# Optimization experiments

Measured on AMD Instinct MI355X. Metric: run time of the kernel, lower is better.

Reference implementation:

```python
import jax, jax.numpy as jnp
import numpy as np

IN_DIM, HID, NCLS = 384, 16, 2
BN_EPS = 1e-5

def setup_inputs() -> dict:
    key = jax.random.key(0)
    ks = jax.random.split(key, 10)
    N, E, G = 50000, 200000, 64
    x = jax.random.normal(ks[0], (N, IN_DIM), dtype=jnp.float32)
    edge_index = jax.random.randint(ks[1], (2, E), 0, N, dtype=jnp.int64)
    batch = jnp.sort(jax.random.randint(ks[2], (N,), 0, G, dtype=jnp.int64))
    s1 = 1.0 / np.sqrt(2 * IN_DIM)
    s2 = 1.0 / np.sqrt(IN_DIM)
    s3 = 1.0 / np.sqrt(HID)
    lin_l_w = jax.random.uniform(ks[3], (HID, 2 * IN_DIM), minval=-s1, maxval=s1, dtype=jnp.float32)
    lin_l_b = jax.random.uniform(ks[4], (HID,), minval=-s1, maxval=s1, dtype=jnp.float32)
    lin_r_w = jax.random.uniform(ks[5], (HID, IN_DIM), minval=-s2, maxval=s2, dtype=jnp.float32)
    bn_gamma = jnp.ones((HID,), dtype=jnp.float32)
    bn_beta = jnp.zeros((HID,), dtype=jnp.float32)
    fc_w = jax.random.uniform(ks[6], (NCLS, HID), minval=-s3, maxval=s3, dtype=jnp.float32)
    fc_b = jax.random.uniform(ks[7], (NCLS,), minval=-s3, maxval=s3, dtype=jnp.float32)
    return {"x": x, "edge_index": edge_index, "batch": batch, "num_graphs": G,
            "lin_l_w": lin_l_w, "lin_l_b": lin_l_b, "lin_r_w": lin_r_w,
            "bn_gamma": bn_gamma, "bn_beta": bn_beta, "fc_w": fc_w, "fc_b": fc_b}

def reference(x, edge_index, batch, num_graphs, lin_l_w, lin_l_b, lin_r_w, bn_gamma, bn_beta, fc_w, fc_b):
    N = x.shape[0]
    # flow='target_to_source': aggregate x[edge_index[1]] (j) onto edge_index[0] (i)
    i, j = edge_index[0], edge_index[1]
    msg = x[j]                                                    # [E, IN_DIM]
    sum_agg = jax.ops.segment_sum(msg, i, num_segments=N)        # [N, IN_DIM]
    cnt = jax.ops.segment_sum(jnp.ones((msg.shape[0],), x.dtype), i, num_segments=N)
    mean_agg = sum_agg / jnp.clip(cnt, 1.0)[:, None]
    max_agg = jax.ops.segment_max(msg, i, num_segments=N)        # -inf where empty
    max_agg = jnp.where(jnp.isfinite(max_agg), max_agg, 0.0)     # PyG leaves 0 for isolated nodes
    agg = jnp.concatenate([mean_agg, max_agg], axis=-1)          # [N, 2*IN_DIM] (MultiAggregation cat)
    h = agg @ lin_l_w.T + lin_l_b + x @ lin_r_w.T                # SAGEConv: lin_l(aggr) + lin_r(root)
    # BatchNorm1d, training-mode batch statistics (biased variance)
    mu = jnp.mean(h, axis=0)
    var = jnp.mean(jnp.square(h - mu), axis=0)
    h = (h - mu) * jax.lax.rsqrt(var + BN_EPS) * bn_gamma + bn_beta
    h = jax.nn.relu(h)                                           # [N, HID]; hierarchical cat of 1 layer = h
    # global_mean_pool
    pooled_sum = jax.ops.segment_sum(h, batch, num_segments=num_graphs)
    gcnt = jax.ops.segment_sum(jnp.ones((N,), h.dtype), batch, num_segments=num_graphs)
    pooled = pooled_sum / jnp.clip(gcnt, 1.0)[:, None]           # [G, HID]
    return pooled @ fc_w.T + fc_b                                # [G, NCLS]
```

## Files before the change

### kernel.cpp

```cpp
#include <hip/hip_runtime.h>
#include <hip/hip_bf16.h>
#include <math.h>

#define IN_DIM 384
#define HID 16
#define NCLS 2
#define BN_EPS 1e-5f
#define MAXG 64
#define SLOTS 64

#define LOF(u) __uint_as_float((u) << 16)
#define HIF(u) __uint_as_float((u) & 0xffff0000u)

typedef __attribute__((ext_vector_type(8))) short bf16x8;
typedef __attribute__((ext_vector_type(4))) float f32x4;

__device__ __forceinline__ unsigned packbf(float a, float b) {
    __hip_bfloat162 h2 = __float22bfloat162_rn(make_float2(a, b));
    union { __hip_bfloat162 h; unsigned u; } c;
    c.h = h2;
    return c.u;
}

__global__ __launch_bounds__(256) void k_scatproj(const int* __restrict__ ei,
                                                  const int* __restrict__ ej, int E,
                                                  int* __restrict__ cnt,
                                                  int* __restrict__ colidx, int sblocks,
                                                  const float* __restrict__ x,
                                                  const float* __restrict__ wl,
                                                  const float* __restrict__ wr,
                                                  int N, float* __restrict__ y,
                                                  unsigned* __restrict__ xb) {
    if ((int)blockIdx.x < sblocks) {
        int e = blockIdx.x * 256 + threadIdx.x;
        if (e < E) {
            int i = ei[e];
            int pos = atomicAdd(&cnt[i], 1);
            if (pos < SLOTS) colidx[(size_t)i * SLOTS + pos] = ej[e];
        }
        return;
    }
    int lane = threadIdx.x & 63;
    int tile = (blockIdx.x - sblocks) * 4 + (threadIdx.x >> 6);
    int ntiles = (N + 15) >> 4;
    if (tile >= ntiles) return;
    int row = lane & 15;
    int g = lane >> 4;
    int node = tile * 16 + row;
    int nodec = min(node, N - 1);
    bool ok = (node < N);
    const float* xr = x + (size_t)nodec * IN_DIM + g * 8;
    const float* wmr = wl + (size_t)row * (2 * IN_DIM) + g * 8;
    const float* wrr = wr + (size_t)row * IN_DIM + g * 8;
    uint4* xo = (uint4*)(xb + (size_t)nodec * 192 + g * 4);
    f32x4 acc0 = {0.f, 0.f, 0.f, 0.f};
    f32x4 acc1 = {0.f, 0.f, 0.f, 0.f};
#pragma unroll
    for (int c = 0; c < 12; c++) {
        float4 xa = *(const float4*)(xr + c * 32);
        float4 xc = *(const float4*)(xr + c * 32 + 4);
        float4 ma = *(const float4*)(wmr + c * 32);
        float4 mc = *(const float4*)(wmr + c * 32 + 4);
        float4 ra = *(const float4*)(wrr + c * 32);
        float4 rc = *(const float4*)(wrr + c * 32 + 4);
        union { uint4 u; bf16x8 v; } xf, wa, wb;
        xf.u.x = packbf(xa.x, xa.y);
        xf.u.y = packbf(xa.z, xa.w);
        xf.u.z = packbf(xc.x, xc.y);
        xf.u.w = packbf(xc.z, xc.w);
        wa.u.x = packbf(ma.x, ma.y);
        wa.u.y = packbf(ma.z, ma.w);
        wa.u.z = packbf(mc.x, mc.y);
        wa.u.w = packbf(mc.z, mc.w);
        wb.u.x = packbf(ra.x, ra.y);
        wb.u.y = packbf(ra.z, ra.w);
        wb.u.z = packbf(rc.x, rc.y);
        wb.u.w = packbf(rc.z, rc.w);
        if (ok) xo[c * 4] = xf.u;
        acc0 = __builtin_amdgcn_mfma_f32_16x16x32_bf16(wa.v, xf.v, acc0, 0, 0, 0);
        acc1 = __builtin_amdgcn_mfma_f32_16x16x32_bf16(wb.v, xf.v, acc1, 0, 0, 0);
    }
    if (ok) {
        float* yo = y + (size_t)node * 32 + g * 4;
        *(float4*)yo = make_float4(acc0[0], acc0[1], acc0[2], acc0[3]);
        *(float4*)(yo + 16) = make_float4(acc1[0], acc1[1], acc1[2], acc1[3]);
    }
}

__global__ __launch_bounds__(256) void k_node(const unsigned* __restrict__ xb,
                                              const float* __restrict__ y,
                                              const float* __restrict__ wl,
                                              const float* __restrict__ lb,
                                              const int* __restrict__ cnt,
                                              const int* __restrict__ colidx, int N,
                                              float* __restrict__ h,
                                              float* __restrict__ stats) {
    __shared__ float shS[32];
    if (threadIdx.x < 32) shS[threadIdx.x] = 0.f;
    __syncthreads();
    int lane = threadIdx.x & 63;
    int wid = threadIdx.x >> 6;
    int kq = ((lane >> 4) << 2) + (lane & 3);
    int nq = (lane & 15) >> 2;
    int slot = lane >> 4;
    int ch = lane & 15;
    float sAcc = 0.f, s2Acc = 0.f;
    int ngroups = (N + 3) >> 2;
    int g = blockIdx.x * 4 + wid;
    if (g < ngroups) {
        int ibase = g << 2;
        int jpre[4];
        int dgv[4];
#pragma unroll
        for (int n = 0; n < 4; n++) {
            int i = ibase + n;
            dgv[n] = (i < N) ? min(cnt[i], SLOTS) : 0;
        }
#pragma unroll
        for (int n = 0; n < 4; n++) {
            int i = ibase + n;
            jpre[n] = (dgv[n] > 0) ? colidx[(size_t)i * SLOTS + min(lane, dgv[n] - 1)] : 0;
        }
        float2 mx[4][3];
        float sd[4];
#pragma unroll
        for (int n = 0; n < 4; n++) {
            int dg = dgv[n];
            float2 m0 = make_float2(-INFINITY, -INFINITY), m1 = m0, m2 = m0;
            float s = 0.f;
            int jv = jpre[n];
            for (int eb = 0; eb < dg; eb += 4) {
                int j0 = __shfl(jv, eb, 64);
                int j1 = __shfl(jv, eb + 1, 64);
                int j2 = __shfl(jv, eb + 2, 64);
                int j3 = __shfl(jv, eb + 3, 64);
                const unsigned* q0 = xb + (size_t)j0 * 192 + lane;
                const unsigned* q1 = xb + (size_t)j1 * 192 + lane;
                const unsigned* q2 = xb + (size_t)j2 * 192 + lane;
                const unsigned* q3 = xb + (size_t)j3 * 192 + lane;
                unsigned a0 = q0[0], a1 = q0[64], a2 = q0[128];
                unsigned b0 = q1[0], b1 = q1[64], b2 = q1[128];
                unsigned c0 = q2[0], c1 = q2[64], c2 = q2[128];
                unsigned d0 = q3[0], d1 = q3[64], d2 = q3[128];
                int js = (slot == 0) ? j0 : (slot == 1) ? j1 : (slot == 2) ? j2 : j3;
                float yv = y[(size_t)js * 32 + ch];
                s += (eb + slot < dg) ? yv : 0.f;
                m0.x = fmaxf(fmaxf(m0.x, fmaxf(LOF(a0), LOF(b0))), fmaxf(LOF(c0), LOF(d0)));
                m0.y = fmaxf(fmaxf(m0.y, fmaxf(HIF(a0), HIF(b0))), fmaxf(HIF(c0), HIF(d0)));
                m1.x = fmaxf(fmaxf(m1.x, fmaxf(LOF(a1), LOF(b1))), fmaxf(LOF(c1), LOF(d1)));
                m1.y = fmaxf(fmaxf(m1.y, fmaxf(HIF(a1), HIF(b1))), fmaxf(HIF(c1), HIF(d1)));
                m2.x = fmaxf(fmaxf(m2.x, fmaxf(LOF(a2), LOF(b2))), fmaxf(LOF(c2), LOF(d2)));
                m2.y = fmaxf(fmaxf(m2.y, fmaxf(HIF(a2), HIF(b2))), fmaxf(HIF(c2), HIF(d2)));
            }
            if (dgv[n] == 0) {
                m0 = make_float2(0.f, 0.f); m1 = m0; m2 = m0;
            }
            mx[n][0] = m0; mx[n][1] = m1; mx[n][2] = m2;
            sd[n] = s;
        }
#pragma unroll
        for (int n = 0; n < 4; n++) {
            sd[n] += __shfl_xor(sd[n], 16, 64);
            sd[n] += __shfl_xor(sd[n], 32, 64);
        }
        const float* wp = wl + IN_DIM + 2 * lane;
        float outv = 0.f;
#pragma unroll
        for (int kg = 0; kg < 4; kg++) {
            float r[16];
#pragma unroll
            for (int kk = 0; kk < 4; kk++) {
                int k = (kg << 2) + kk;
                const float* wrow = wp + (size_t)k * (2 * IN_DIM);
                float2 w0 = *(const float2*)wrow;
                float2 w1 = *(const float2*)(wrow + 128);
                float2 w2 = *(const float2*)(wrow + 256);
#pragma unroll
                for (int n = 0; n < 4; n++) {
                    float t = mx[n][0].x * w0.x;
                    t = fmaf(mx[n][0].y, w0.y, t);
                    t = fmaf(mx[n][1].x, w1.x, t);
                    t = fmaf(mx[n][1].y, w1.y, t);
                    t = fmaf(mx[n][2].x, w2.x, t);
                    t = fmaf(mx[n][2].y, w2.y, t);
                    r[(n << 2) + kk] = t;
                }
            }
#pragma unroll
            for (int st = 0; st < 4; st++) {
                int step = 1 << st;
                bool hi = (lane & step) != 0;
#pragma unroll
                for (int m = 0; m < (8 >> st); m++) {
                    float a = r[2 * m], b = r[2 * m + 1];
                    float send = hi ? a : b;
                    float keep = hi ? b : a;
                    r[m] = keep + __shfl_xor(send, step, 64);
                }
            }
            float v = r[0];
            v += __shfl_xor(v, 16, 64);
            v += __shfl_xor(v, 32, 64);
            if ((lane >> 4) == kg) outv = v;
        }
        int iw = ibase + nq;
        float t0 = __shfl(sd[0], kq, 64), t1 = __shfl(sd[1], kq, 64);
        float t2 = __shfl(sd[2], kq, 64), t3 = __shfl(sd[3], kq, 64);
        float sv = (nq == 0) ? t0 : (nq == 1) ? t1 : (nq == 2) ? t2 : t3;
        int dgs = (nq == 0) ? dgv[0] : (nq == 1) ? dgv[1] : (nq == 2) ? dgv[2] : dgv[3];
        if (iw < N) {
            float mean = sv / (float)max(dgs, 1);
            float hv = mean + outv + y[(size_t)iw * 32 + 16 + kq] + lb[kq];
            h[(size_t)iw * HID + kq] = hv;
            sAcc += hv;
            s2Acc = fmaf(hv, hv, s2Acc);
        }
    }
    __syncthreads();
    atomicAdd(&shS[kq], sAcc);
    atomicAdd(&shS[16 + kq], s2Acc);
    __syncthreads();
    if (threadIdx.x < 32) atomicAdd(&stats[threadIdx.x], shS[threadIdx.x]);
}

__global__ __launch_bounds__(256) void k_pool(const float* __restrict__ h,
                                              const int* __restrict__ batch,
                                              const float* __restrict__ stats,
                                              const float* __restrict__ gamma,
                                              const float* __restrict__ beta, int N,
                                              float* __restrict__ pooled,
                                              int* __restrict__ gcnt,
                                              int* __restrict__ ticket,
                                              const float* __restrict__ fcw,
                                              const float* __restrict__ fcb, int G,
                                              float* __restrict__ out) {
    __shared__ float smP[MAXG * HID];
    __shared__ int smC[MAXG];
    __shared__ int isLast;
    for (int idx = threadIdx.x; idx < MAXG * HID; idx += blockDim.x) smP[idx] = 0.f;
    if (threadIdx.x < MAXG) smC[threadIdx.x] = 0;
    __syncthreads();
    int c = threadIdx.x & 15;
    float invN = 1.f / (float)N;
    float mu = stats[c] * invN;
    float var = stats[16 + c] * invN - mu * mu;
    float sc = gamma[c] * rsqrtf(var + BN_EPS);
    float sh = beta[c] - mu * sc;
    int base = blockIdx.x * 256;
    int endn = min(base + 256, N);
    for (int idx = base * HID + threadIdx.x; idx < endn * HID; idx += blockDim.x) {
        int n = idx >> 4;
        float v = fmaxf(fmaf(h[idx], sc, sh), 0.f);
        int g = batch[n] & (MAXG - 1);
        atomicAdd(&smP[g * HID + c], v);
        if (c == 0) atomicAdd(&smC[g], 1);
    }
    __syncthreads();
    for (int idx = threadIdx.x; idx < MAXG * HID; idx += blockDim.x)
        if (smP[idx] != 0.f) atomicAdd(&pooled[idx], smP[idx]);
    if (threadIdx.x < MAXG && smC[threadIdx.x]) atomicAdd(&gcnt[threadIdx.x], smC[threadIdx.x]);
    __threadfence();
    __syncthreads();
    if (threadIdx.x == 0) {
        int t = atomicAdd(ticket, 1);
        isLast = (t == (int)gridDim.x - 1);
    }
    __syncthreads();
    if (isLast && threadIdx.x < G) {
        int g = threadIdx.x;
        __threadfence();
        int cntg = atomicAdd(&gcnt[g], 0);
        float inv = 1.f / (float)max(cntg, 1);
        float o0 = fcb[0], o1 = fcb[1];
#pragma unroll
        for (int chh = 0; chh < HID; chh++) {
            float pv = atomicAdd(&pooled[g * HID + chh], 0.f) * inv;
            o0 = fmaf(pv, fcw[chh], o0);
            o1 = fmaf(pv, fcw[HID + chh], o1);
        }
        out[g * NCLS + 0] = o0;
        out[g * NCLS + 1] = o1;
    }
}

extern "C" void kernel_launch(void* const* d_in, const int* in_sizes, int n_in,
                              void* d_out, int out_size, void* d_ws, size_t ws_size,
                              hipStream_t stream) {
    const float* x = (const float*)d_in[0];
    const int* ei = (const int*)d_in[1];
    const int* batch = (const int*)d_in[2];
    const float* wl = (const float*)d_in[4];
    const float* lb = (const float*)d_in[5];
    const float* wr = (const float*)d_in[6];
    const float* gamma = (const float*)d_in[7];
    const float* beta = (const float*)d_in[8];
    const float* fcw = (const float*)d_in[9];
    const float* fcb = (const float*)d_in[10];

    const int N = in_sizes[0] / IN_DIM;
    const int E = in_sizes[1] / 2;
    const int G = out_size / NCLS;
    const int* ej = ei + E;

    size_t off = 0;
    auto take = [&](size_t b) { size_t r = off; off += (b + 255) & ~(size_t)255; return r; };
    size_t cnt_off  = take((size_t)N * 4);
    size_t stat_off = take(32 * 4);
    size_t pool_off = take((size_t)MAXG * HID * 4);
    size_t gcnt_off = take((size_t)MAXG * 4);
    size_t tick_off = take(4);
    size_t zero_bytes = off;
    size_t col_off  = take((size_t)N * SLOTS * 4);
    size_t y_off    = take((size_t)N * 32 * 4);
    size_t h_off    = take((size_t)N * HID * 4);
    size_t xb_off   = take((size_t)N * 192 * 4 + 4096);
    (void)ws_size;

    char* ws = (char*)d_ws;
    int* cnt = (int*)(ws + cnt_off);
    float* stats = (float*)(ws + stat_off);
    float* pooled = (float*)(ws + pool_off);
    int* gcnt = (int*)(ws + gcnt_off);
    int* ticket = (int*)(ws + tick_off);
    int* colidx = (int*)(ws + col_off);
    float* y = (float*)(ws + y_off);
    float* h = (float*)(ws + h_off);
    unsigned* xb = (unsigned*)(ws + xb_off);

    hipMemsetAsync(d_ws, 0, zero_bytes, stream);

    int eblocks = (E + 255) / 256;
    int ngroups = (N + 3) >> 2;
    int gblocks = (ngroups + 3) / 4;
    int ntiles = (N + 15) >> 4;
    int pblocks = (ntiles + 3) / 4;
    k_scatproj<<<eblocks + pblocks, 256, 0, stream>>>(ei, ej, E, cnt, colidx, eblocks,
                                                      x, wl, wr, N, y, xb);
    k_node<<<gblocks, 256, 0, stream>>>(xb, y, wl, lb, cnt, colidx, N, h, stats);
    k_pool<<<(N + 255) / 256, 256, 0, stream>>>(h, batch, stats, gamma, beta, N, pooled,
                                                gcnt, ticket, fcw, fcb, G, (float*)d_out);
}
```

Baseline: 140.1 us.

## Drop bf16 copy of x; gather fp32 rows directly for max aggregation

Removes the bf16 staging buffer of x that the projection kernel wrote, so the neighbor max-gather in k_node now reads fp32 rows of x directly. The projection kernel now handles two 16-node tiles per wave, reusing the converted weight fragments across both tiles. This removes a 38MB write and the extra launch-side buffer, but doubles the bytes read per gathered neighbor (fp32 instead of bf16), trading write traffic for heavier random gather traffic.

```diff
diff --git a/kernel.cpp b/kernel.cpp
--- a/kernel.cpp
+++ b/kernel.cpp
@@ -8,9 +8,6 @@
 #define BN_EPS 1e-5f
 #define MAXG 64
 #define SLOTS 64
-
-#define LOF(u) __uint_as_float((u) << 16)
-#define HIF(u) __uint_as_float((u) & 0xffff0000u)
 
 typedef __attribute__((ext_vector_type(8))) short bf16x8;
 typedef __attribute__((ext_vector_type(4))) float f32x4;
@@ -29,8 +26,7 @@
                                                   const float* __restrict__ x,
                                                   const float* __restrict__ wl,
                                                   const float* __restrict__ wr,
-                                                  int N, float* __restrict__ y,
-                                                  unsigned* __restrict__ xb) {
+                                                  int N, float* __restrict__ y) {
     if ((int)blockIdx.x < sblocks) {
         int e = blockIdx.x * 256 + threadIdx.x;
         if (e < E) {
@@ -41,53 +37,60 @@
         return;
     }
     int lane = threadIdx.x & 63;
-    int tile = (blockIdx.x - sblocks) * 4 + (threadIdx.x >> 6);
     int ntiles = (N + 15) >> 4;
-    if (tile >= ntiles) return;
+    int npairs = (ntiles + 1) >> 1;
+    int pair = (blockIdx.x - sblocks) * 4 + (threadIdx.x >> 6);
+    if (pair >= npairs) return;
+    int t0 = pair * 2;
+    int t1 = min(t0 + 1, ntiles - 1);
+    bool two = (t0 + 1 < ntiles);
     int row = lane & 15;
     int g = lane >> 4;
-    int node = tile * 16 + row;
-    int nodec = min(node, N - 1);
-    bool ok = (node < N);
-    const float* xr = x + (size_t)nodec * IN_DIM + g * 8;
+    int node0 = t0 * 16 + row, node1 = t1 * 16 + row;
+    int nc0 = min(node0, N - 1), nc1 = min(node1, N - 1);
+    bool ok0 = (node0 < N), ok1 = two && (node1 < N);
+    const float* xr0 = x + (size_t)nc0 * IN_DIM + g * 8;
+    const float* xr1 = x + (size_t)nc1 * IN_DIM + g * 8;
     const float* wmr = wl + (size_t)row * (2 * IN_DIM) + g * 8;
     const float* wrr = wr + (size_t)row * IN_DIM + g * 8;
-    uint4* xo = (uint4*)(xb + (size_t)nodec * 192 + g * 4);
-    f32x4 acc0 = {0.f, 0.f, 0.f, 0.f};
-    f32x4 acc1 = {0.f, 0.f, 0.f, 0.f};
+    f32x4 a0m = {0.f, 0.f, 0.f, 0.f}, a0r = a0m, a1m = a0m, a1r = a0m;
 #pragma unroll
     for (int c = 0; c < 12; c++) {
-        float4 xa = *(const float4*)(xr + c * 32);
-        float4 xc = *(const float4*)(xr + c * 32 + 4);
         float4 ma = *(const float4*)(wmr + c * 32);
         float4 mc = *(const float4*)(wmr + c * 32 + 4);
         float4 ra = *(const float4*)(wrr + c * 32);
         float4 rc = *(const float4*)(wrr + c * 32 + 4);
-        union { uint4 u; bf16x8 v; } xf, wa, wb;
-        xf.u.x = packbf(xa.x, xa.y);
-        xf.u.y = packbf(xa.z, xa.w);
-        xf.u.z = packbf(xc.x, xc.y);
-        xf.u.w = packbf(xc.z, xc.w);
-        wa.u.x = packbf(ma.x, ma.y);
-        wa.u.y = packbf(ma.z, ma.w);
-        wa.u.z = packbf(mc.x, mc.y);
-        wa.u.w = packbf(mc.z, mc.w);
-        wb.u.x = packbf(ra.x, ra.y);
-        wb.u.y = packbf(ra.z, ra.w);
-        wb.u.z = packbf(rc.x, rc.y);
-        wb.u.w = packbf(rc.z, rc.w);
-        if (ok) xo[c * 4] = xf.u;
-        acc0 = __builtin_amdgcn_mfma_f32_16x16x32_bf16(wa.v, xf.v, acc0, 0, 0, 0);
-        acc1 = __builtin_amdgcn_mfma_f32_16x16x32_bf16(wb.v, xf.v, acc1, 0, 0, 0);
-    }
-    if (ok) {
-        float* yo = y + (size_t)node * 32 + g * 4;
-        *(float4*)yo = make_float4(acc0[0], acc0[1], acc0[2], acc0[3]);
-        *(float4*)(yo + 16) = make_float4(acc1[0], acc1[1], acc1[2], acc1[3]);
-    }
-}
-
-__global__ __launch_bounds__(256) void k_node(const unsigned* __restrict__ xb,
+        float4 p0 = *(const float4*)(xr0 + c * 32);
+        float4 q0 = *(const float4*)(xr0 + c * 32 + 4);
+        float4 p1 = *(const float4*)(xr1 + c * 32);
+        float4 q1 = *(const float4*)(xr1 + c * 32 + 4);
+        union { uint4 u; bf16x8 v; } wa, wb, x0, x1;
+        wa.u.x = packbf(ma.x, ma.y); wa.u.y = packbf(ma.z, ma.w);
+        wa.u.z = packbf(mc.x, mc.y); wa.u.w = packbf(mc.z, mc.w);
+        wb.u.x = packbf(ra.x, ra.y); wb.u.y = packbf(ra.z, ra.w);
+        wb.u.z = packbf(rc.x, rc.y); wb.u.w = packbf(rc.z, rc.w);
+        x0.u.x = packbf(p0.x, p0.y); x0.u.y = packbf(p0.z, p0.w);
+        x0.u.z = packbf(q0.x, q0.y); x0.u.w = packbf(q0.z, q0.w);
+        x1.u.x = packbf(p1.x, p1.y); x1.u.y = packbf(p1.z, p1.w);
+        x1.u.z = packbf(q1.x, q1.y); x1.u.w = packbf(q1.z, q1.w);
+        a0m = __builtin_amdgcn_mfma_f32_16x16x32_bf16(wa.v, x0.v, a0m, 0, 0, 0);
+        a0r = __builtin_amdgcn_mfma_f32_16x16x32_bf16(wb.v, x0.v, a0r, 0, 0, 0);
+        a1m = __builtin_amdgcn_mfma_f32_16x16x32_bf16(wa.v, x1.v, a1m, 0, 0, 0);
+        a1r = __builtin_amdgcn_mfma_f32_16x16x32_bf16(wb.v, x1.v, a1r, 0, 0, 0);
+    }
+    if (ok0) {
+        float* yo = y + (size_t)node0 * 32 + g * 4;
+        *(float4*)yo = make_float4(a0m[0], a0m[1], a0m[2], a0m[3]);
+        *(float4*)(yo + 16) = make_float4(a0r[0], a0r[1], a0r[2], a0r[3]);
+    }
+    if (ok1) {
+        float* yo = y + (size_t)node1 * 32 + g * 4;
+        *(float4*)yo = make_float4(a1m[0], a1m[1], a1m[2], a1m[3]);
+        *(float4*)(yo + 16) = make_float4(a1r[0], a1r[1], a1r[2], a1r[3]);
+    }
+}
+
+__global__ __launch_bounds__(256) void k_node(const float* __restrict__ x,
                                               const float* __restrict__ y,
                                               const float* __restrict__ wl,
                                               const float* __restrict__ lb,
@@ -104,6 +107,7 @@
     int nq = (lane & 15) >> 2;
     int slot = lane >> 4;
     int ch = lane & 15;
+    const float* xl = x + 2 * lane;
     float sAcc = 0.f, s2Acc = 0.f;
     int ngroups = (N + 3) >> 2;
     int g = blockIdx.x * 4 + wid;
@@ -134,25 +138,29 @@
                 int j1 = __shfl(jv, eb + 1, 64);
                 int j2 = __shfl(jv, eb + 2, 64);
                 int j3 = __shfl(jv, eb + 3, 64);
-                const unsigned* q0 = xb + (size_t)j0 * 192 + lane;
-                const unsigned* q1 = xb + (size_t)j1 * 192 + lane;
-                const unsigned* q2 = xb + (size_t)j2 * 192 + lane;
-                const unsigned* q3 = xb + (size_t)j3 * 192 + lane;
-                unsigned a0 = q0[0], a1 = q0[64], a2 = q0[128];
-                unsigned b0 = q1[0], b1 = q1[64], b2 = q1[128];
-                unsigned c0 = q2[0], c1 = q2[64], c2 = q2[128];
-                unsigned d0 = q3[0], d1 = q3[64], d2 = q3[128];
+                const float* p0 = xl + (size_t)j0 * IN_DIM;
+                const float* p1 = xl + (size_t)j1 * IN_DIM;
+                const float* p2 = xl + (size_t)j2 * IN_DIM;
+                const float* p3 = xl + (size_t)j3 * IN_DIM;
+                float2 a00 = *(const float2*)p0, a01 = *(const float2*)(p0 + 128),
+                       a02 = *(const float2*)(p0 + 256);
+                float2 a10 = *(const float2*)p1, a11 = *(const float2*)(p1 + 128),
+                       a12 = *(const float2*)(p1 + 256);
+                float2 a20 = *(const float2*)p2, a21 = *(const float2*)(p2 + 128),
+                       a22 = *(const float2*)(p2 + 256);
+                float2 a30 = *(const float2*)p3, a31 = *(const float2*)(p3 + 128),
+                       a32 = *(const float2*)(p3 + 256);
                 int js = (slot == 0) ? j0 : (slot == 1) ? j1 : (slot == 2) ? j2 : j3;
                 float yv = y[(size_t)js * 32 + ch];
                 s += (eb + slot < dg) ? yv : 0.f;
-                m0.x = fmaxf(fmaxf(m0.x, fmaxf(LOF(a0), LOF(b0))), fmaxf(LOF(c0), LOF(d0)));
-                m0.y = fmaxf(fmaxf(m0.y, fmaxf(HIF(a0), HIF(b0))), fmaxf(HIF(c0), HIF(d0)));
-                m1.x = fmaxf(fmaxf(m1.x, fmaxf(LOF(a1), LOF(b1))), fmaxf(LOF(c1), LOF(d1)));
-                m1.y = fmaxf(fmaxf(m1.y, fmaxf(HIF(a1), HIF(b1))), fmaxf(HIF(c1), HIF(d1)));
-                m2.x = fmaxf(fmaxf(m2.x, fmaxf(LOF(a2), LOF(b2))), fmaxf(LOF(c2), LOF(d2)));
-                m2.y = fmaxf(fmaxf(m2.y, fmaxf(HIF(a2), HIF(b2))), fmaxf(HIF(c2), HIF(d2)));
+                m0.x = fmaxf(fmaxf(m0.x, fmaxf(a00.x, a10.x)), fmaxf(a20.x, a30.x));
+                m0.y = fmaxf(fmaxf(m0.y, fmaxf(a00.y, a10.y)), fmaxf(a20.y, a30.y));
+                m1.x = fmaxf(fmaxf(m1.x, fmaxf(a01.x, a11.x)), fmaxf(a21.x, a31.x));
+                m1.y = fmaxf(fmaxf(m1.y, fmaxf(a01.y, a11.y)), fmaxf(a21.y, a31.y));
+                m2.x = fmaxf(fmaxf(m2.x, fmaxf(a02.x, a12.x)), fmaxf(a22.x, a32.x));
+                m2.y = fmaxf(fmaxf(m2.y, fmaxf(a02.y, a12.y)), fmaxf(a22.y, a32.y));
             }
-            if (dgv[n] == 0) {
+            if (dg == 0) {
                 m0 = make_float2(0.f, 0.f); m1 = m0; m2 = m0;
             }
             mx[n][0] = m0; mx[n][1] = m1; mx[n][2] = m2;
@@ -313,7 +321,6 @@
     size_t col_off  = take((size_t)N * SLOTS * 4);
     size_t y_off    = take((size_t)N * 32 * 4);
     size_t h_off    = take((size_t)N * HID * 4);
-    size_t xb_off   = take((size_t)N * 192 * 4 + 4096);
     (void)ws_size;
 
     char* ws = (char*)d_ws;
@@ -325,7 +332,6 @@
     int* colidx = (int*)(ws + col_off);
     float* y = (float*)(ws + y_off);
     float* h = (float*)(ws + h_off);
-    unsigned* xb = (unsigned*)(ws + xb_off);
 
     hipMemsetAsync(d_ws, 0, zero_bytes, stream);
 
@@ -333,10 +339,11 @@
     int ngroups = (N + 3) >> 2;
     int gblocks = (ngroups + 3) / 4;
     int ntiles = (N + 15) >> 4;
-    int pblocks = (ntiles + 3) / 4;
+    int npairs = (ntiles + 1) >> 1;
+    int pblocks = (npairs + 3) / 4;
     k_scatproj<<<eblocks + pblocks, 256, 0, stream>>>(ei, ej, E, cnt, colidx, eblocks,
-                                                      x, wl, wr, N, y, xb);
-    k_node<<<gblocks, 256, 0, stream>>>(xb, y, wl, lb, cnt, colidx, N, h, stats);
+                                                      x, wl, wr, N, y);
+    k_node<<<gblocks, 256, 0, stream>>>(x, y, wl, lb, cnt, colidx, N, h, stats);
     k_pool<<<(N + 255) / 256, 256, 0, stream>>>(h, batch, stats, gamma, beta, N, pooled,
                                                 gcnt, ticket, fcw, fcb, G, (float*)d_out);
 }
```

Measured after the change: 130.7 us (median of 2 runs). -6.7%, faster.
